# Performance work log

Measured on AMD Instinct MI355X. Metric: run time of the kernel, lower is better.

## Reference

```python
import jax, jax.numpy as jnp
import numpy as np

N_OUT = 100_000   # destination (output) nodes
N_IN = 200_000    # source nodes (x_feat rows); first N_OUT are the self/dst nodes
DEG = 16          # sample_count / fixed fan-out
E = N_OUT * DEG   # edges
D_IN = 128
D_OUT = 128


def setup_inputs() -> dict:
    key = jax.random.key(0)
    k1, k2, k3 = jax.random.split(key, 3)
    x_feat = jax.random.normal(k1, (N_IN, D_IN), dtype=jnp.float32)
    # MFG CSR with fixed fan-out DEG (what make_mfg_csr(sample_size=DEG) encodes)
    csr_row_ptr = jnp.arange(N_OUT + 1, dtype=jnp.int64) * DEG
    csr_col_ind = jax.random.randint(k2, (E,), 0, N_IN, dtype=jnp.int64)
    # Linear(2*D_IN, D_OUT) with xavier_uniform(gain for relu) weight
    gain = float(np.sqrt(2.0))
    fan_in, fan_out = 2 * D_IN, D_OUT
    bound = gain * float(np.sqrt(6.0 / (fan_in + fan_out)))
    W = jax.random.uniform(k3, (D_OUT, 2 * D_IN), dtype=jnp.float32,
                           minval=-bound, maxval=bound)
    lin_bias = jnp.zeros((D_OUT,), dtype=jnp.float32)
    bias = jnp.zeros((D_OUT,), dtype=jnp.float32)  # extra additive Parameter
    return {"x_feat": x_feat, "csr_row_ptr": csr_row_ptr,
            "csr_col_ind": csr_col_ind, "sample_count": DEG,
            "W": W, "lin_bias": lin_bias, "bias": bias}


def _segment_ids(row_ptr, n_edges):
    # seg[e] = destination row of edge e; handles empty rows via duplicate adds
    ones = jnp.zeros((n_edges,), dtype=jnp.int32).at[row_ptr[1:-1]].add(1)
    return jnp.cumsum(ones)


def reference(x_feat, csr_row_ptr, csr_col_ind, sample_count, W, lin_bias, bias):
    n_out = csr_row_ptr.shape[0] - 1
    n_edges = csr_col_ind.shape[0]
    seg = _segment_ids(csr_row_ptr, n_edges)
    # mean aggregation over sampled neighbors (cugraphops agg 'mean')
    gathered = x_feat[csr_col_ind]                          # [E, D_IN]
    summed = jax.ops.segment_sum(gathered, seg, num_segments=n_out)
    deg = (csr_row_ptr[1:] - csr_row_ptr[:-1]).astype(x_feat.dtype)
    mean_agg = summed / jnp.maximum(deg, 1.0)[:, None]      # [n_out, D_IN]
    # concat self (dst) features with aggregated features, then Linear
    x_agg = jnp.concatenate([x_feat[:n_out], mean_agg], axis=-1)  # [n_out, 2*D_IN]
    y = x_agg @ W.T + lin_bias + bias
    return y
```

## Files before the change

kernel.cpp:

```cpp
#include <hip/hip_runtime.h>
#include <hip/hip_bf16.h>

#define D 128
#define K2 256
#define NT 64
#define NTHREADS 256
#define AGM_LD 136
#define WT_LD 68

typedef __attribute__((ext_vector_type(8))) short bf16x8;
typedef __attribute__((ext_vector_type(4))) float f32x4;
typedef __attribute__((ext_vector_type(2))) float f32x2;
typedef __attribute__((ext_vector_type(4))) float f32x4v;

static __device__ __forceinline__ unsigned short f2bf(float f) {
    __hip_bfloat16 h = __float2bfloat16(f);
    return *reinterpret_cast<unsigned short*>(&h);
}

static __device__ __forceinline__ unsigned int f2q_manual(float f) {
    f = fminf(fmaxf(f, -448.f), 448.f);
    unsigned int u = __float_as_uint(f * 0x1.0p-120f);
    const unsigned int lsb = (u >> 20) & 1u;
    u += 0x7ffffu + lsb;
    return ((u >> 24) & 0x80u) | ((u >> 20) & 0x7fu);
}
static __device__ __forceinline__ float q2f_manual(unsigned int b) {
    const unsigned int bits = ((b & 0x80u) << 24) | ((b & 0x7fu) << 20);
    return __uint_as_float(bits) * 0x1.0p+120f;
}
static __device__ __forceinline__ unsigned int pack_fp8x4(f32x4v v) {
#if __has_builtin(__builtin_amdgcn_cvt_pk_fp8_f32)
    int lo = __builtin_amdgcn_cvt_pk_fp8_f32(v.x, v.y, 0, false);
    int q  = __builtin_amdgcn_cvt_pk_fp8_f32(v.z, v.w, lo, true);
    return (unsigned int)q;
#else
    return f2q_manual(v.x) | (f2q_manual(v.y) << 8) |
           (f2q_manual(v.z) << 16) | (f2q_manual(v.w) << 24);
#endif
}
static __device__ __forceinline__ f32x2 unpack_fp8_lo(unsigned int v) {
#if __has_builtin(__builtin_amdgcn_cvt_pk_f32_fp8)
    return __builtin_amdgcn_cvt_pk_f32_fp8((int)v, false);
#else
    f32x2 r; r[0] = q2f_manual(v & 0xffu); r[1] = q2f_manual((v >> 8) & 0xffu); return r;
#endif
}
static __device__ __forceinline__ f32x2 unpack_fp8_hi(unsigned int v) {
#if __has_builtin(__builtin_amdgcn_cvt_pk_f32_fp8)
    return __builtin_amdgcn_cvt_pk_f32_fp8((int)v, true);
#else
    f32x2 r; r[0] = q2f_manual((v >> 16) & 0xffu); r[1] = q2f_manual((v >> 24) & 0xffu); return r;
#endif
}

__global__ __launch_bounds__(256)
void convert_all(const float* __restrict__ x, const float* __restrict__ W,
                 unsigned int* __restrict__ xq4,
                 uint2* __restrict__ xbs4,
                 uint2* __restrict__ wb4,
                 long n4x, long n4s, long n4w)
{
    const long gid = (long)blockIdx.x * blockDim.x + threadIdx.x;
    const long stride = (long)gridDim.x * blockDim.x;
    for (long t = gid; t < n4x; t += stride) {
        const f32x4v v = __builtin_nontemporal_load(
            &reinterpret_cast<const f32x4v*>(x)[t]);
        xq4[t] = pack_fp8x4(v);
        if (t < n4s) {
            uint2 p;
            p.x = (unsigned int)f2bf(v.x) | ((unsigned int)f2bf(v.y) << 16);
            p.y = (unsigned int)f2bf(v.z) | ((unsigned int)f2bf(v.w) << 16);
            xbs4[t] = p;
        }
    }
    for (long t = gid; t < n4w; t += stride) {
        const f32x4v v = __builtin_nontemporal_load(
            &reinterpret_cast<const f32x4v*>(W)[t]);
        uint2 p;
        p.x = (unsigned int)f2bf(v.x) | ((unsigned int)f2bf(v.y) << 16);
        p.y = (unsigned int)f2bf(v.z) | ((unsigned int)f2bf(v.w) << 16);
        wb4[t] = p;
    }
}

__global__ __launch_bounds__(NTHREADS, 4)
void sage_fp8b(const unsigned char* __restrict__ xq,
               const unsigned short* __restrict__ xbs,
               const unsigned short* __restrict__ wb,
               const int* __restrict__ rp,
               const int* __restrict__ ci,
               const float* __restrict__ lb,
               const float* __restrict__ bb,
               float* __restrict__ y,
               int n_out)
{
    __shared__ unsigned short aggM[NT][AGM_LD];
    __shared__ unsigned short wtT[D][WT_LD];
    __shared__ int rpls[NT + 1];
    __shared__ int cils[NT * 16];

    const int tid   = threadIdx.x;
    const int wave  = tid >> 6;
    const int lane  = tid & 63;
    const int node0 = blockIdx.x * NT;
    const int nt_act = min(NT, n_out - node0);

    if (tid <= nt_act) rpls[tid] = rp[node0 + tid];
    __syncthreads();
    const int e_base = rpls[0];
    const int e_cnt  = rpls[nt_act] - e_base;
    const bool fits  = (e_cnt <= NT * 16);
    if (fits) {
        for (int i = tid; i < e_cnt; i += NTHREADS) cils[i] = ci[e_base + i];
    }
    __syncthreads();

    const int nsel = lane >> 5;
    const int dg4  = (lane & 31) * 4;

    for (int p = 0; p < 8; ++p) {
        const int n0 = wave * 16 + p * 2;
        if (n0 >= nt_act) break;
        const bool has1 = (n0 + 1 < nt_act);

        const int s0 = rpls[n0] - e_base;
        const int d0 = rpls[n0 + 1] - e_base - s0;
        int s1 = s0, d1 = d0;
        if (has1) { s1 = rpls[n0 + 1] - e_base; d1 = rpls[n0 + 2] - e_base - s1; }

        const int  my_n   = n0 + nsel;
        const int  my_s   = nsel ? s1 : s0;
        const int  my_d   = nsel ? d1 : d0;
        const bool active = (nsel == 0) || has1;

        f32x2 a01 = (f32x2){0.f, 0.f};
        f32x2 a23 = (f32x2){0.f, 0.f};
        if (fits && has1 && d0 == 16 && d1 == 16) {
            int idx[16];
            #pragma unroll
            for (int u = 0; u < 16; ++u) idx[u] = cils[my_s + u];
            #pragma unroll
            for (int u = 0; u < 16; ++u) {
                const unsigned int v = *reinterpret_cast<const unsigned int*>(
                    &xq[(size_t)idx[u] * D + dg4]);
                a01 += unpack_fp8_lo(v);
                a23 += unpack_fp8_hi(v);
            }
        } else if (active) {
            for (int u = 0; u < my_d; ++u) {
                const int c = fits ? cils[my_s + u] : ci[e_base + my_s + u];
                const unsigned int v = *reinterpret_cast<const unsigned int*>(
                    &xq[(size_t)c * D + dg4]);
                a01 += unpack_fp8_lo(v);
                a23 += unpack_fp8_hi(v);
            }
        }
        if (active) {
            const float inv = 1.0f / (float)max(my_d, 1);
            uint2 pk;
            pk.x = (unsigned int)f2bf(a01[0] * inv) | ((unsigned int)f2bf(a01[1] * inv) << 16);
            pk.y = (unsigned int)f2bf(a23[0] * inv) | ((unsigned int)f2bf(a23[1] * inv) << 16);
            *reinterpret_cast<uint2*>(&aggM[my_n][dg4]) = pk;
        }
    }

    const int n15 = lane & 15;
    const int g   = lane >> 4;

    const int arow = min(node0 + wave * 16 + n15, n_out - 1);
    bf16x8 aself[4];
    #pragma unroll
    for (int c = 0; c < 4; ++c)
        aself[c] = *reinterpret_cast<const bf16x8*>(
            &xbs[(size_t)arow * D + c * 32 + g * 8]);

    f32x4 acc[8];
    #pragma unroll
    for (int f = 0; f < 8; ++f) acc[f] = (f32x4){0.f, 0.f, 0.f, 0.f};

    #pragma unroll
    for (int ch = 0; ch < 4; ++ch) {
        const int k0 = ch * 64;
        #pragma unroll
        for (int j = 0; j < 8; ++j) {
            const int flat = j * 256 + tid;
            const int o    = flat >> 4;
            const int q    = flat & 15;
            *reinterpret_cast<uint2*>(&wtT[o][q * 4]) =
                *reinterpret_cast<const uint2*>(&wb[(size_t)o * K2 + k0 + q * 4]);
        }
        __syncthreads();

        #pragma unroll
        for (int sub = 0; sub < 2; ++sub) {
            const int kk = k0 + sub * 32;
            const bf16x8 a = (kk < 128)
                ? aself[ch * 2 + sub]
                : *reinterpret_cast<const bf16x8*>(
                      &aggM[wave * 16 + n15][(kk - 128) + g * 8]);
            #pragma unroll
            for (int f = 0; f < 8; ++f) {
                const bf16x8 b = *reinterpret_cast<const bf16x8*>(
                    &wtT[f * 16 + n15][sub * 32 + g * 8]);
                acc[f] = __builtin_amdgcn_mfma_f32_16x16x32_bf16(a, b, acc[f], 0, 0, 0);
            }
        }
        __syncthreads();
    }

    const int mbase = node0 + wave * 16 + g * 4;
    #pragma unroll
    for (int f = 0; f < 8; ++f) {
        const int col  = f * 16 + n15;
        const float bs = lb[col] + bb[col];
        #pragma unroll
        for (int r = 0; r < 4; ++r) {
            const int row = mbase + r;
            if (row < n_out)
                __builtin_nontemporal_store(acc[f][r] + bs, &y[(size_t)row * D + col]);
        }
    }
}

#define AGG_LDF 264
__global__ __launch_bounds__(NTHREADS, 3)
void sage_fused3(const float* __restrict__ x,
                 const int* __restrict__ rp,
                 const int* __restrict__ ci,
                 const float* __restrict__ W,
                 const float* __restrict__ lb,
                 const float* __restrict__ bb,
                 float* __restrict__ y,
                 int n_out)
{
    __shared__ unsigned short aggB[NT][AGG_LDF];
    __shared__ unsigned short wtTF[D][32];
    __shared__ int rplsF[NT + 1];
    __shared__ int cilsF[NT * 16];

    const int tid   = threadIdx.x;
    const int wave  = tid >> 6;
    const int lane  = tid & 63;
    const int node0 = blockIdx.x * NT;
    const int nt_act = min(NT, n_out - node0);

    if (tid <= nt_act) rplsF[tid] = rp[node0 + tid];
    __syncthreads();
    const int e_base = rplsF[0];
    const int e_cnt  = rplsF[nt_act] - e_base;
    const bool fits  = (e_cnt <= NT * 16);
    if (fits) {
        for (int i = tid; i < e_cnt; i += NTHREADS) cilsF[i] = ci[e_base + i];
    }
    __syncthreads();

    for (int t = 0; t < 16; ++t) {
        const int nn = wave * 16 + t;
        if (nn >= nt_act) break;
        const int node = node0 + nn;
        const float2 self =
            *reinterpret_cast<const float2*>(&x[(size_t)node * D + lane * 2]);
        const int s  = rplsF[nn] - e_base;
        const int dg = rplsF[nn + 1] - e_base - s;
        float ax = 0.f, ay = 0.f;
        for (int u = 0; u < dg; ++u) {
            const int c = fits ? cilsF[s + u] : ci[e_base + s + u];
            const float2 v = *reinterpret_cast<const float2*>(
                &x[(size_t)c * D + lane * 2]);
            ax += v.x; ay += v.y;
        }
        const float inv = 1.0f / (float)max(dg, 1);
        *reinterpret_cast<unsigned int*>(&aggB[nn][lane * 2]) =
            (unsigned int)f2bf(self.x) | ((unsigned int)f2bf(self.y) << 16);
        *reinterpret_cast<unsigned int*>(&aggB[nn][D + lane * 2]) =
            (unsigned int)f2bf(ax * inv) | ((unsigned int)f2bf(ay * inv) << 16);
    }

    const int n15 = lane & 15;
    const int g   = lane >> 4;
    f32x4 acc[8];
    #pragma unroll
    for (int f = 0; f < 8; ++f) acc[f] = (f32x4){0.f, 0.f, 0.f, 0.f};

    for (int k0 = 0; k0 < K2; k0 += 32) {
        #pragma unroll
        for (int j = 0; j < 4; ++j) {
            const int idx = j * 256 + tid;
            const int o   = idx >> 3;
            const int c   = idx & 7;
            const float4 w = *reinterpret_cast<const float4*>(
                &W[(size_t)o * K2 + k0 + c * 4]);
            const unsigned int lo = (unsigned int)f2bf(w.x) | ((unsigned int)f2bf(w.y) << 16);
            const unsigned int hi = (unsigned int)f2bf(w.z) | ((unsigned int)f2bf(w.w) << 16);
            *reinterpret_cast<uint2*>(&wtTF[o][c * 4]) = make_uint2(lo, hi);
        }
        __syncthreads();
        const bf16x8 a = *reinterpret_cast<const bf16x8*>(
            &aggB[wave * 16 + n15][k0 + g * 8]);
        #pragma unroll
        for (int f = 0; f < 8; ++f) {
            const bf16x8 b = *reinterpret_cast<const bf16x8*>(&wtTF[f * 16 + n15][g * 8]);
            acc[f] = __builtin_amdgcn_mfma_f32_16x16x32_bf16(a, b, acc[f], 0, 0, 0);
        }
        __syncthreads();
    }

    const int mbase = node0 + wave * 16 + g * 4;
    #pragma unroll
    for (int f = 0; f < 8; ++f) {
        const int col  = f * 16 + n15;
        const float bs = lb[col] + bb[col];
        #pragma unroll
        for (int r = 0; r < 4; ++r) {
            const int row = mbase + r;
            if (row < n_out)
                y[(size_t)row * D + col] = acc[f][r] + bs;
        }
    }
}

extern "C" void kernel_launch(void* const* d_in, const int* in_sizes, int n_in,
                              void* d_out, int out_size, void* d_ws, size_t ws_size,
                              hipStream_t stream)
{
    const float* x  = (const float*)d_in[0];
    const int*   rp = (const int*)d_in[1];
    const int*   ci = (const int*)d_in[2];
    const float* W  = (const float*)d_in[4];
    const float* lb = (const float*)d_in[5];
    const float* bb = (const float*)d_in[6];
    float* y = (float*)d_out;

    const int n_out = in_sizes[1] - 1;
    const int grid  = (n_out + NT - 1) / NT;

    const size_t n_x = (size_t)in_sizes[0];
    const size_t n_w = (size_t)in_sizes[4];
    const size_t xq_bytes  = n_x;
    const size_t xbs_bytes = (size_t)n_out * D * 2;
    const size_t wb_bytes  = n_w * 2;
    const size_t need = xq_bytes + xbs_bytes + wb_bytes;

    if (ws_size >= need) {
        unsigned char*  xq  = (unsigned char*)d_ws;
        unsigned short* xbs = (unsigned short*)((char*)d_ws + xq_bytes);
        unsigned short* wb  = (unsigned short*)((char*)d_ws + xq_bytes + xbs_bytes);
        hipLaunchKernelGGL(convert_all, dim3(2048), dim3(256), 0, stream,
                           x, W, (unsigned int*)xq, (uint2*)xbs, (uint2*)wb,
                           (long)(n_x >> 2), (long)(((size_t)n_out * D) >> 2),
                           (long)(n_w >> 2));
        hipLaunchKernelGGL(sage_fp8b, dim3(grid), dim3(NTHREADS), 0, stream,
                           xq, xbs, wb, rp, ci, lb, bb, y, n_out);
    } else {
        hipLaunchKernelGGL(sage_fused3, dim3(grid), dim3(NTHREADS), 0, stream,
                           x, rp, ci, W, lb, bb, y, n_out);
    }
}
```

Before: 81.02 us.

## Restructure fp8 SAGE kernel: 8 waves, register-resident W slices, no weight LDS staging

The main kernel moves to 512 threads (8 waves). Each wave now aggregates 8 nodes and, in the GEMM phase, owns a 16-column slice of the output whose bf16 weight fragments are loaded straight from global memory into registers. This replaces the chunked LDS transpose of W and its four barrier pairs. Self features are staged into LDS next to the aggregated means, so every wave reads A tiles from LDS across all 64 rows. The convert kernel also drops its nontemporal loads and the output drops its nontemporal stores. The trade-off is one extra LDS buffer and more registers per thread, which could limit occupancy at the higher thread count.

```diff
diff --git a/kernel.cpp b/kernel.cpp
--- a/kernel.cpp
+++ b/kernel.cpp
@@ -4,14 +4,12 @@
 #define D 128
 #define K2 256
 #define NT 64
-#define NTHREADS 256
+#define NTHREADS 512
 #define AGM_LD 136
-#define WT_LD 68
 
 typedef __attribute__((ext_vector_type(8))) short bf16x8;
 typedef __attribute__((ext_vector_type(4))) float f32x4;
 typedef __attribute__((ext_vector_type(2))) float f32x2;
-typedef __attribute__((ext_vector_type(4))) float f32x4v;
 
 static __device__ __forceinline__ unsigned short f2bf(float f) {
     __hip_bfloat16 h = __float2bfloat16(f);
@@ -29,7 +27,7 @@
     const unsigned int bits = ((b & 0x80u) << 24) | ((b & 0x7fu) << 20);
     return __uint_as_float(bits) * 0x1.0p+120f;
 }
-static __device__ __forceinline__ unsigned int pack_fp8x4(f32x4v v) {
+static __device__ __forceinline__ unsigned int pack_fp8x4(float4 v) {
 #if __has_builtin(__builtin_amdgcn_cvt_pk_fp8_f32)
     int lo = __builtin_amdgcn_cvt_pk_fp8_f32(v.x, v.y, 0, false);
     int q  = __builtin_amdgcn_cvt_pk_fp8_f32(v.z, v.w, lo, true);
@@ -64,8 +62,7 @@
     const long gid = (long)blockIdx.x * blockDim.x + threadIdx.x;
     const long stride = (long)gridDim.x * blockDim.x;
     for (long t = gid; t < n4x; t += stride) {
-        const f32x4v v = __builtin_nontemporal_load(
-            &reinterpret_cast<const f32x4v*>(x)[t]);
+        const float4 v = reinterpret_cast<const float4*>(x)[t];
         xq4[t] = pack_fp8x4(v);
         if (t < n4s) {
             uint2 p;
@@ -75,8 +72,7 @@
         }
     }
     for (long t = gid; t < n4w; t += stride) {
-        const f32x4v v = __builtin_nontemporal_load(
-            &reinterpret_cast<const f32x4v*>(W)[t]);
+        const float4 v = reinterpret_cast<const float4*>(W)[t];
         uint2 p;
         p.x = (unsigned int)f2bf(v.x) | ((unsigned int)f2bf(v.y) << 16);
         p.y = (unsigned int)f2bf(v.z) | ((unsigned int)f2bf(v.w) << 16);
@@ -84,8 +80,8 @@
     }
 }
 
-__global__ __launch_bounds__(NTHREADS, 4)
-void sage_fp8b(const unsigned char* __restrict__ xq,
+__global__ __launch_bounds__(NTHREADS, 6)
+void sage_fp8r(const unsigned char* __restrict__ xq,
                const unsigned short* __restrict__ xbs,
                const unsigned short* __restrict__ wb,
                const int* __restrict__ rp,
@@ -95,8 +91,8 @@
                float* __restrict__ y,
                int n_out)
 {
+    __shared__ unsigned short aggS[NT][AGM_LD];
     __shared__ unsigned short aggM[NT][AGM_LD];
-    __shared__ unsigned short wtT[D][WT_LD];
     __shared__ int rpls[NT + 1];
     __shared__ int cils[NT * 16];
 
@@ -119,8 +115,8 @@
     const int nsel = lane >> 5;
     const int dg4  = (lane & 31) * 4;
 
-    for (int p = 0; p < 8; ++p) {
-        const int n0 = wave * 16 + p * 2;
+    for (int p = 0; p < 4; ++p) {
+        const int n0 = wave * 8 + p * 2;
         if (n0 >= nt_act) break;
         const bool has1 = (n0 + 1 < nt_act);
 
@@ -133,6 +129,12 @@
         const int  my_s   = nsel ? s1 : s0;
         const int  my_d   = nsel ? d1 : d0;
         const bool active = (nsel == 0) || has1;
+
+        if (active) {
+            const uint2 sv = *reinterpret_cast<const uint2*>(
+                &xbs[(size_t)(node0 + my_n) * D + dg4]);
+            *reinterpret_cast<uint2*>(&aggS[my_n][dg4]) = sv;
+        }
 
         f32x2 a01 = (f32x2){0.f, 0.f};
         f32x2 a23 = (f32x2){0.f, 0.f};
@@ -165,66 +167,49 @@
         }
     }
 
-    const int n15 = lane & 15;
-    const int g   = lane >> 4;
-
-    const int arow = min(node0 + wave * 16 + n15, n_out - 1);
-    bf16x8 aself[4];
-    #pragma unroll
-    for (int c = 0; c < 4; ++c)
-        aself[c] = *reinterpret_cast<const bf16x8*>(
-            &xbs[(size_t)arow * D + c * 32 + g * 8]);
-
-    f32x4 acc[8];
-    #pragma unroll
-    for (int f = 0; f < 8; ++f) acc[f] = (f32x4){0.f, 0.f, 0.f, 0.f};
-
-    #pragma unroll
-    for (int ch = 0; ch < 4; ++ch) {
-        const int k0 = ch * 64;
-        #pragma unroll
-        for (int j = 0; j < 8; ++j) {
-            const int flat = j * 256 + tid;
-            const int o    = flat >> 4;
-            const int q    = flat & 15;
-            *reinterpret_cast<uint2*>(&wtT[o][q * 4]) =
-                *reinterpret_cast<const uint2*>(&wb[(size_t)o * K2 + k0 + q * 4]);
-        }
-        __syncthreads();
-
-        #pragma unroll
-        for (int sub = 0; sub < 2; ++sub) {
-            const int kk = k0 + sub * 32;
-            const bf16x8 a = (kk < 128)
-                ? aself[ch * 2 + sub]
-                : *reinterpret_cast<const bf16x8*>(
-                      &aggM[wave * 16 + n15][(kk - 128) + g * 8]);
-            #pragma unroll
-            for (int f = 0; f < 8; ++f) {
-                const bf16x8 b = *reinterpret_cast<const bf16x8*>(
-                    &wtT[f * 16 + n15][sub * 32 + g * 8]);
-                acc[f] = __builtin_amdgcn_mfma_f32_16x16x32_bf16(a, b, acc[f], 0, 0, 0);
-            }
-        }
-        __syncthreads();
-    }
-
-    const int mbase = node0 + wave * 16 + g * 4;
-    #pragma unroll
-    for (int f = 0; f < 8; ++f) {
-        const int col  = f * 16 + n15;
-        const float bs = lb[col] + bb[col];
+    const int n15  = lane & 15;
+    const int g    = lane >> 4;
+    const int colb = wave * 16;
+
+    bf16x8 Bf[8];
+    #pragma unroll
+    for (int kc = 0; kc < 8; ++kc)
+        Bf[kc] = *reinterpret_cast<const bf16x8*>(
+            &wb[(size_t)(colb + n15) * K2 + kc * 32 + g * 8]);
+
+    __syncthreads();
+
+    f32x4 acc[4];
+    #pragma unroll
+    for (int mt = 0; mt < 4; ++mt) acc[mt] = (f32x4){0.f, 0.f, 0.f, 0.f};
+
+    #pragma unroll
+    for (int mt = 0; mt < 4; ++mt) {
+        const int arow = mt * 16 + n15;
+        #pragma unroll
+        for (int kc = 0; kc < 8; ++kc) {
+            const bf16x8 a = (kc < 4)
+                ? *reinterpret_cast<const bf16x8*>(&aggS[arow][kc * 32 + g * 8])
+                : *reinterpret_cast<const bf16x8*>(&aggM[arow][(kc - 4) * 32 + g * 8]);
+            acc[mt] = __builtin_amdgcn_mfma_f32_16x16x32_bf16(a, Bf[kc], acc[mt], 0, 0, 0);
+        }
+    }
+
+    const int col = colb + n15;
+    const float bs = lb[col] + bb[col];
+    #pragma unroll
+    for (int mt = 0; mt < 4; ++mt) {
         #pragma unroll
         for (int r = 0; r < 4; ++r) {
-            const int row = mbase + r;
+            const int row = node0 + mt * 16 + g * 4 + r;
             if (row < n_out)
-                __builtin_nontemporal_store(acc[f][r] + bs, &y[(size_t)row * D + col]);
+                y[(size_t)row * D + col] = acc[mt][r] + bs;
         }
     }
 }
 
 #define AGG_LDF 264
-__global__ __launch_bounds__(NTHREADS, 3)
+__global__ __launch_bounds__(256, 3)
 void sage_fused3(const float* __restrict__ x,
                  const int* __restrict__ rp,
                  const int* __restrict__ ci,
@@ -251,7 +236,7 @@
     const int e_cnt  = rplsF[nt_act] - e_base;
     const bool fits  = (e_cnt <= NT * 16);
     if (fits) {
-        for (int i = tid; i < e_cnt; i += NTHREADS) cilsF[i] = ci[e_base + i];
+        for (int i = tid; i < e_cnt; i += 256) cilsF[i] = ci[e_base + i];
     }
     __syncthreads();
 
@@ -350,10 +335,10 @@
                            x, W, (unsigned int*)xq, (uint2*)xbs, (uint2*)wb,
                            (long)(n_x >> 2), (long)(((size_t)n_out * D) >> 2),
                            (long)(n_w >> 2));
-        hipLaunchKernelGGL(sage_fp8b, dim3(grid), dim3(NTHREADS), 0, stream,
+        hipLaunchKernelGGL(sage_fp8r, dim3(grid), dim3(NTHREADS), 0, stream,
                            xq, xbs, wb, rp, ci, lb, bb, y, n_out);
     } else {
-        hipLaunchKernelGGL(sage_fused3, dim3(grid), dim3(NTHREADS), 0, stream,
+        hipLaunchKernelGGL(sage_fused3, dim3(grid), dim3(256), 0, stream,
                            x, rp, ci, W, lb, bb, y, n_out);
     }
 }
```

Measured after the change: 75.27 us. 1.08x faster.
